# Performance work log

Hardware: AMD Instinct MI355X
Metric: run time of the kernel (lower is better)

## Reference

```python
import jax, jax.numpy as jnp
import numpy as np

HIDDEN = 64

def setup_inputs() -> dict:
    key = jax.random.key(0)
    ks = jax.random.split(key, 8)
    B, T, D, O, H = 1024, 256, 128, 128, HIDDEN
    s_ih = 1.0 / np.sqrt(H)
    inp = {
        "x": jax.random.normal(ks[0], (B, T, D), dtype=jnp.float32),
        "W_ih": jax.random.uniform(ks[1], (4 * H, D), jnp.float32, -s_ih, s_ih),
        "W_hh": jax.random.uniform(ks[2], (4 * H, H), jnp.float32, -s_ih, s_ih),
        "b_ih": jax.random.uniform(ks[3], (4 * H,), jnp.float32, -s_ih, s_ih),
        "b_hh": jax.random.uniform(ks[4], (4 * H,), jnp.float32, -s_ih, s_ih),
        "W_o": jax.random.uniform(ks[5], (O, H), jnp.float32, -s_ih, s_ih),
        "b_o": jax.random.uniform(ks[6], (O,), jnp.float32, -s_ih, s_ih),
    }
    return inp

def _lstm_last_h(x, W_ih, W_hh, b_ih, b_hh):
    # x: [B, T, D]. PyTorch gate order: i, f, g, o.
    B, T, D = x.shape
    H = HIDDEN
    # Precompute input contribution for all steps: [T, B, 4H]
    gx = jnp.einsum('btd,gd->tbg', x, W_ih) + (b_ih + b_hh)

    def step(carry, gx_t):
        h, c = carry
        gates = gx_t + h @ W_hh.T  # [B, 4H]
        i = jax.nn.sigmoid(gates[:, 0 * H:1 * H])
        f = jax.nn.sigmoid(gates[:, 1 * H:2 * H])
        g = jnp.tanh(gates[:, 2 * H:3 * H])
        o = jax.nn.sigmoid(gates[:, 3 * H:4 * H])
        c = f * c + i * g
        h = o * jnp.tanh(c)
        return (h, c), None

    h0 = jnp.zeros((B, H), x.dtype)
    c0 = jnp.zeros((B, H), x.dtype)
    (h_T, _), _ = jax.lax.scan(step, (h0, c0), gx)
    return h_T  # [B, H] == output[:, -1, :]

def reference(x, W_ih, W_hh, b_ih, b_hh, W_o, b_o):
    h = _lstm_last_h(x, W_ih, W_hh, b_ih, b_hh)
    logits = jax.nn.relu(h) @ W_o.T + b_o  # [B, O]; dropout is identity in eval
    return jax.nn.log_softmax(logits, axis=1)
```

## Files before the change

kernel.cpp:

```cpp
#include <hip/hip_runtime.h>
#include <math.h>

constexpr int B = 1024, T = 256, D = 128, H = 64, O = 128;
constexpr int BQ = 16;
constexpr int NBLK = B / BQ;
constexpr int TC = 8;
constexpr int NCH = T / TC;

typedef __attribute__((ext_vector_type(8))) short short8;
typedef __attribute__((ext_vector_type(4))) float f32x4;

__device__ __forceinline__ unsigned short f2bf(float f) {
    union { float f; unsigned u; } v; v.f = f;
    return (unsigned short)((v.u + 0x7FFF + ((v.u >> 16) & 1)) >> 16);
}
__device__ __forceinline__ float frcp(float x) { return __builtin_amdgcn_rcpf(x); }
__device__ __forceinline__ float sigmoidf_(float x) {
    return frcp(1.0f + __expf(-x));
}
__device__ __forceinline__ float tanhf_(float x) {
    return fmaf(2.0f, frcp(1.0f + __expf(-2.0f * x)), -1.0f);
}
__device__ __forceinline__ void lds_barrier() {
    asm volatile("s_waitcnt lgkmcnt(0)\n\ts_barrier" ::: "memory");
}

__global__ __launch_bounds__(256, 1)
void lstm_fused(const float* __restrict__ x, const float* __restrict__ Wih,
                const float* __restrict__ Whh, const float* __restrict__ bih,
                const float* __restrict__ bhh, const float* __restrict__ Wo,
                const float* __restrict__ bo, float* __restrict__ out)
{
    __shared__ unsigned short xfrag[2][TC][4 * 64 * 8];
    __shared__ unsigned short hfrag[2][2 * 64 * 8];
    __shared__ float hf[BQ][H];

    const int tid  = threadIdx.x;
    const int lane = tid & 63;
    const int w    = tid >> 6;
    const int lq   = lane & 15;
    const int qd   = lane >> 4;
    const int b0   = blockIdx.x * BQ;

    short8 wih_f[4][4];
    short8 whh_f[4][2];
    float  bias[4];
    #pragma unroll
    for (int q = 0; q < 4; ++q) {
        const int n = 64 * q + 16 * w + lq;
        #pragma unroll
        for (int c = 0; c < 4; ++c) {
            const float* p = Wih + (size_t)n * D + 32 * c + 8 * qd;
            short8 v;
            #pragma unroll
            for (int j = 0; j < 8; ++j) v[j] = (short)f2bf(p[j]);
            wih_f[q][c] = v;
        }
        #pragma unroll
        for (int c = 0; c < 2; ++c) {
            const float* p = Whh + (size_t)n * H + 32 * c + 8 * qd;
            short8 v;
            #pragma unroll
            for (int j = 0; j < 8; ++j) v[j] = (short)f2bf(p[j]);
            whh_f[q][c] = v;
        }
        bias[q] = bih[n] + bhh[n];
    }

    const int ms    = tid >> 4;
    const int kslot = tid & 15;
    const int c_p   = kslot >> 2;
    const int q_p   = kslot & 3;
    const int l_p   = (q_p << 4) | ms;
    const int xoff  = c_p * 1024 + ((l_p * 16) ^ (c_p * 32));
    const float* xrow = x + (size_t)(b0 + ms) * T * D + 8 * kslot;

    int xro[4], hro[2];
    #pragma unroll
    for (int c = 0; c < 4; ++c) xro[c] = c * 1024 + ((lane * 16) ^ (c * 32));
    #pragma unroll
    for (int c = 0; c < 2; ++c) hro[c] = c * 1024 + lane * 16;

    const int hrow_base = (w >> 1) * 512 +
                          (16 * ((2 * w + (lq >> 3)) & 3) + 4 * qd) * 8 + (lq & 7);

    *(short8*)&hfrag[0][tid * 8 * 2 / 2 - tid * 8 + tid * 8] = short8{0,0,0,0,0,0,0,0};
    *(short8*)&hfrag[0][tid * 4] = short8{0,0,0,0,0,0,0,0};
    *(short8*)&hfrag[1][tid * 4] = short8{0,0,0,0,0,0,0,0};

    float4 pf[16];
    #pragma unroll
    for (int tt = 0; tt < TC; ++tt) {
        const float* p = xrow + (size_t)tt * D;
        pf[2 * tt]     = *(const float4*)p;
        pf[2 * tt + 1] = *(const float4*)(p + 4);
    }
    #pragma unroll
    for (int tt = 0; tt < TC; ++tt) {
        float4 a = pf[2 * tt], bv = pf[2 * tt + 1];
        short8 v;
        v[0] = (short)f2bf(a.x);  v[1] = (short)f2bf(a.y);
        v[2] = (short)f2bf(a.z);  v[3] = (short)f2bf(a.w);
        v[4] = (short)f2bf(bv.x); v[5] = (short)f2bf(bv.y);
        v[6] = (short)f2bf(bv.z); v[7] = (short)f2bf(bv.w);
        *(short8*)((char*)&xfrag[0][tt][0] + xoff) = v;
    }
    #pragma unroll
    for (int tt = 0; tt < TC; ++tt) {
        const float* p = xrow + (size_t)(TC + tt) * D;
        pf[2 * tt]     = *(const float4*)p;
        pf[2 * tt + 1] = *(const float4*)(p + 4);
    }
    __syncthreads();

    float cst[4] = {0.f, 0.f, 0.f, 0.f};
    float hlast[4];
    int buf = 0;

    for (int ch = 0; ch < NCH; ++ch) {
        #pragma unroll
        for (int tt = 0; tt < TC; ++tt) {
            const int hcur = tt & 1, hnxt = hcur ^ 1;

            short8 xf[4], hfr[2];
            #pragma unroll
            for (int c = 0; c < 4; ++c)
                xf[c] = *(const short8*)((char*)&xfrag[buf][tt][0] + xro[c]);
            #pragma unroll
            for (int c = 0; c < 2; ++c)
                hfr[c] = *(const short8*)((char*)&hfrag[hcur][0] + hro[c]);

            f32x4 acc[4];
            #pragma unroll
            for (int q = 0; q < 4; ++q) {
                f32x4 a = {bias[q], bias[q], bias[q], bias[q]};
                #pragma unroll
                for (int c = 0; c < 4; ++c)
                    a = __builtin_amdgcn_mfma_f32_16x16x32_bf16(xf[c], wih_f[q][c], a, 0, 0, 0);
                #pragma unroll
                for (int c = 0; c < 2; ++c)
                    a = __builtin_amdgcn_mfma_f32_16x16x32_bf16(hfr[c], whh_f[q][c], a, 0, 0, 0);
                acc[q] = a;
            }

            #pragma unroll
            for (int r = 0; r < 4; ++r) {
                float gi = sigmoidf_(acc[0][r]);
                float gf = sigmoidf_(acc[1][r]);
                float gg = tanhf_  (acc[2][r]);
                float go = sigmoidf_(acc[3][r]);
                float c2 = fmaf(gf, cst[r], gi * gg);
                cst[r] = c2;
                float hv = go * tanhf_(c2);
                hlast[r] = hv;
                hfrag[hnxt][hrow_base + r * 8] = f2bf(hv);
            }

            lds_barrier();
        }

        if (ch + 1 < NCH) {
            const int nb = buf ^ 1;
            #pragma unroll
            for (int tt = 0; tt < TC; ++tt) {
                float4 a = pf[2 * tt], bv = pf[2 * tt + 1];
                short8 v;
                v[0] = (short)f2bf(a.x);  v[1] = (short)f2bf(a.y);
                v[2] = (short)f2bf(a.z);  v[3] = (short)f2bf(a.w);
                v[4] = (short)f2bf(bv.x); v[5] = (short)f2bf(bv.y);
                v[6] = (short)f2bf(bv.z); v[7] = (short)f2bf(bv.w);
                *(short8*)((char*)&xfrag[nb][tt][0] + xoff) = v;
            }
            const int ch2 = (ch + 2 < NCH) ? ch + 2 : NCH - 1;
            #pragma unroll
            for (int tt = 0; tt < TC; ++tt) {
                const float* p = xrow + ((size_t)ch2 * TC + tt) * D;
                pf[2 * tt]     = *(const float4*)p;
                pf[2 * tt + 1] = *(const float4*)(p + 4);
            }
            lds_barrier();
            buf = nb;
        }
    }

    #pragma unroll
    for (int r = 0; r < 4; ++r) hf[4 * qd + r][16 * w + lq] = hlast[r];
    __syncthreads();

    for (int it = 0; it < 4; ++it) {
        const int m = 4 * it + w;
        float l0 = bo[lane], l1 = bo[lane + 64];
        const float* w0 = Wo + (size_t)lane * H;
        const float* w1 = Wo + (size_t)(lane + 64) * H;
        #pragma unroll
        for (int k = 0; k < H; ++k) {
            float rh = fmaxf(hf[m][k], 0.0f);
            l0 += rh * w0[k];
            l1 += rh * w1[k];
        }
        float mx = fmaxf(l0, l1);
        #pragma unroll
        for (int sh = 32; sh > 0; sh >>= 1) mx = fmaxf(mx, __shfl_xor(mx, sh));
        float e = __expf(l0 - mx) + __expf(l1 - mx);
        #pragma unroll
        for (int sh = 32; sh > 0; sh >>= 1) e += __shfl_xor(e, sh);
        float lse = mx + __logf(e);
        float* op = out + (size_t)(b0 + m) * O;
        op[lane]      = l0 - lse;
        op[lane + 64] = l1 - lse;
    }
}

extern "C" void kernel_launch(void* const* d_in, const int* in_sizes, int n_in,
                              void* d_out, int out_size, void* d_ws, size_t ws_size,
                              hipStream_t stream) {
    const float* x   = (const float*)d_in[0];
    const float* Wih = (const float*)d_in[1];
    const float* Whh = (const float*)d_in[2];
    const float* bih = (const float*)d_in[3];
    const float* bhh = (const float*)d_in[4];
    const float* Wo  = (const float*)d_in[5];
    const float* bo  = (const float*)d_in[6];
    lstm_fused<<<dim3(NBLK), dim3(256), 0, stream>>>(
        x, Wih, Whh, bih, bhh, Wo, bo, (float*)d_out);
}
```

Before: 351.1 us.

## Batch input-projection MFMAs per chunk off the recurrent critical path

The input projection W_ih·x for all 8 timesteps of a chunk is now computed up front into register accumulators (gxacc) at each chunk boundary. Each recurrent step then only issues the h·W_hh MFMAs on top of the precomputed values, which shortens the serial dependency chain per timestep. The x staging buffer becomes single-buffered, with a barrier before the batched projection. The hfrag zero-initialisation is also rewritten to clear the whole buffer. In exchange, register pressure rises substantially (128 extra VGPRs for gxacc), which risks spills.

```diff
diff --git a/kernel.cpp b/kernel.cpp
--- a/kernel.cpp
+++ b/kernel.cpp
@@ -31,7 +31,7 @@
                 const float* __restrict__ bhh, const float* __restrict__ Wo,
                 const float* __restrict__ bo, float* __restrict__ out)
 {
-    __shared__ unsigned short xfrag[2][TC][4 * 64 * 8];
+    __shared__ unsigned short xfrag[TC][4 * 64 * 8];
     __shared__ unsigned short hfrag[2][2 * 64 * 8];
     __shared__ float hf[BQ][H];
 
@@ -84,11 +84,10 @@
     const int hrow_base = (w >> 1) * 512 +
                           (16 * ((2 * w + (lq >> 3)) & 3) + 4 * qd) * 8 + (lq & 7);
 
-    *(short8*)&hfrag[0][tid * 8 * 2 / 2 - tid * 8 + tid * 8] = short8{0,0,0,0,0,0,0,0};
-    *(short8*)&hfrag[0][tid * 4] = short8{0,0,0,0,0,0,0,0};
-    *(short8*)&hfrag[1][tid * 4] = short8{0,0,0,0,0,0,0,0};
-
-    float4 pf[16];
+    for (int i = tid; i < 2 * 2 * 64 * 8 / 2; i += 256)
+        ((unsigned int*)hfrag)[i] = 0;
+
+    float4 pf[2 * TC];
     #pragma unroll
     for (int tt = 0; tt < TC; ++tt) {
         const float* p = xrow + (size_t)tt * D;
@@ -103,7 +102,25 @@
         v[2] = (short)f2bf(a.z);  v[3] = (short)f2bf(a.w);
         v[4] = (short)f2bf(bv.x); v[5] = (short)f2bf(bv.y);
         v[6] = (short)f2bf(bv.z); v[7] = (short)f2bf(bv.w);
-        *(short8*)((char*)&xfrag[0][tt][0] + xoff) = v;
+        *(short8*)((char*)&xfrag[tt][0] + xoff) = v;
+    }
+    __syncthreads();
+
+    f32x4 gxacc[TC][4];
+    #pragma unroll
+    for (int tt = 0; tt < TC; ++tt) {
+        short8 xf[4];
+        #pragma unroll
+        for (int c = 0; c < 4; ++c)
+            xf[c] = *(const short8*)((char*)&xfrag[tt][0] + xro[c]);
+        #pragma unroll
+        for (int q = 0; q < 4; ++q) {
+            f32x4 a = {bias[q], bias[q], bias[q], bias[q]};
+            #pragma unroll
+            for (int c = 0; c < 4; ++c)
+                a = __builtin_amdgcn_mfma_f32_16x16x32_bf16(xf[c], wih_f[q][c], a, 0, 0, 0);
+            gxacc[tt][q] = a;
+        }
     }
     #pragma unroll
     for (int tt = 0; tt < TC; ++tt) {
@@ -111,21 +128,16 @@
         pf[2 * tt]     = *(const float4*)p;
         pf[2 * tt + 1] = *(const float4*)(p + 4);
     }
-    __syncthreads();
 
     float cst[4] = {0.f, 0.f, 0.f, 0.f};
     float hlast[4];
-    int buf = 0;
 
     for (int ch = 0; ch < NCH; ++ch) {
         #pragma unroll
         for (int tt = 0; tt < TC; ++tt) {
             const int hcur = tt & 1, hnxt = hcur ^ 1;
 
-            short8 xf[4], hfr[2];
-            #pragma unroll
-            for (int c = 0; c < 4; ++c)
-                xf[c] = *(const short8*)((char*)&xfrag[buf][tt][0] + xro[c]);
+            short8 hfr[2];
             #pragma unroll
             for (int c = 0; c < 2; ++c)
                 hfr[c] = *(const short8*)((char*)&hfrag[hcur][0] + hro[c]);
@@ -133,10 +145,7 @@
             f32x4 acc[4];
             #pragma unroll
             for (int q = 0; q < 4; ++q) {
-                f32x4 a = {bias[q], bias[q], bias[q], bias[q]};
-                #pragma unroll
-                for (int c = 0; c < 4; ++c)
-                    a = __builtin_amdgcn_mfma_f32_16x16x32_bf16(xf[c], wih_f[q][c], a, 0, 0, 0);
+                f32x4 a = gxacc[tt][q];
                 #pragma unroll
                 for (int c = 0; c < 2; ++c)
                     a = __builtin_amdgcn_mfma_f32_16x16x32_bf16(hfr[c], whh_f[q][c], a, 0, 0, 0);
@@ -160,7 +169,6 @@
         }
 
         if (ch + 1 < NCH) {
-            const int nb = buf ^ 1;
             #pragma unroll
             for (int tt = 0; tt < TC; ++tt) {
                 float4 a = pf[2 * tt], bv = pf[2 * tt + 1];
@@ -169,17 +177,33 @@
                 v[2] = (short)f2bf(a.z);  v[3] = (short)f2bf(a.w);
                 v[4] = (short)f2bf(bv.x); v[5] = (short)f2bf(bv.y);
                 v[6] = (short)f2bf(bv.z); v[7] = (short)f2bf(bv.w);
-                *(short8*)((char*)&xfrag[nb][tt][0] + xoff) = v;
-            }
-            const int ch2 = (ch + 2 < NCH) ? ch + 2 : NCH - 1;
+                *(short8*)((char*)&xfrag[tt][0] + xoff) = v;
+            }
+            {
+                const int ch2 = (ch + 2 < NCH) ? ch + 2 : NCH - 1;
+                #pragma unroll
+                for (int tt = 0; tt < TC; ++tt) {
+                    const float* p = xrow + ((size_t)ch2 * TC + tt) * D;
+                    pf[2 * tt]     = *(const float4*)p;
+                    pf[2 * tt + 1] = *(const float4*)(p + 4);
+                }
+            }
+            lds_barrier();
             #pragma unroll
             for (int tt = 0; tt < TC; ++tt) {
-                const float* p = xrow + ((size_t)ch2 * TC + tt) * D;
-                pf[2 * tt]     = *(const float4*)p;
-                pf[2 * tt + 1] = *(const float4*)(p + 4);
-            }
-            lds_barrier();
-            buf = nb;
+                short8 xf[4];
+                #pragma unroll
+                for (int c = 0; c < 4; ++c)
+                    xf[c] = *(const short8*)((char*)&xfrag[tt][0] + xro[c]);
+                #pragma unroll
+                for (int q = 0; q < 4; ++q) {
+                    f32x4 a = {bias[q], bias[q], bias[q], bias[q]};
+                    #pragma unroll
+                    for (int c = 0; c < 4; ++c)
+                        a = __builtin_amdgcn_mfma_f32_16x16x32_bf16(xf[c], wih_f[q][c], a, 0, 0, 0);
+                    gxacc[tt][q] = a;
+                }
+            }
         }
     }
 
```

Result: no change. 357.7 us (+1.9%).
